# Kernel optimization log

Hardware: AMD Instinct MI355X
Metric: run time of the kernel (lower is better)

## Reference

```python
import jax, jax.numpy as jnp
import numpy as np

B, S, Nv, D, DF, H = 8, 1024, 768, 512, 2048, 8
DH = D // H
EPS = 1e-5


def _layernorm(x, g, b):
    mu = jnp.mean(x, axis=-1, keepdims=True)
    var = jnp.mean((x - mu) ** 2, axis=-1, keepdims=True)
    return (x - mu) * jax.lax.rsqrt(var + EPS) * g + b


def _mha(x, Wq, Wk, Wv, Wo):
    b, s, d = x.shape
    q = (x @ Wq).reshape(b, s, H, DH)
    k = (x @ Wk).reshape(b, s, H, DH)
    v = (x @ Wv).reshape(b, s, H, DH)
    scores = jnp.einsum('bqhd,bkhd->bhqk', q, k) / np.sqrt(DH).astype(np.float32)
    a = jax.nn.softmax(scores, axis=-1)
    o = jnp.einsum('bhqk,bkhd->bqhd', a, v).reshape(b, s, d)
    return o @ Wo


def setup_inputs() -> dict:
    key = jax.random.key(0)
    ks = jax.random.split(key, 20)
    sc = 1.0 / np.sqrt(D)
    scf = 1.0 / np.sqrt(DF)
    n = lambda k, shp, s: (jax.random.normal(k, shp, jnp.float32) * s)
    return {
        'x': n(ks[0], (B, S, D), 1.0),
        'idx_emb_1': jax.random.randint(ks[1], (B, Nv), 0, Nv, dtype=jnp.int64) if jax.config.jax_enable_x64 else jax.random.randint(ks[1], (B, Nv), 0, Nv).astype(jnp.int32),
        'idx_pro_1': jax.random.randint(ks[2], (B, Nv), 0, Nv).astype(jnp.int32),
        'N': Nv,
        'Wq1': n(ks[3], (D, D), sc), 'Wk1': n(ks[4], (D, D), sc),
        'Wv1': n(ks[5], (D, D), sc), 'Wo1': n(ks[6], (D, D), sc),
        'Wq2': n(ks[7], (D, D), sc), 'Wk2': n(ks[8], (D, D), sc),
        'Wv2': n(ks[9], (D, D), sc), 'Wo2': n(ks[10], (D, D), sc),
        'w_conv1': n(ks[11], (D, DF), sc), 'b_conv1': jnp.zeros((DF,), jnp.float32),
        'w_conv2': n(ks[12], (DF, D), scf), 'b_conv2': jnp.zeros((D,), jnp.float32),
        'g1': jnp.ones((D,), jnp.float32), 'beta1': jnp.zeros((D,), jnp.float32),
        'g2': jnp.ones((D,), jnp.float32), 'beta2': jnp.zeros((D,), jnp.float32),
    }


def reference(x, idx_emb_1, idx_pro_1, N,
              Wq1, Wk1, Wv1, Wo1, Wq2, Wk2, Wv2, Wo2,
              w_conv1, b_conv1, w_conv2, b_conv2, g1, beta1, g2, beta2):
    # batched gather-reorder of first N tokens; rest pass through
    x_l1 = x.at[:, :N].set(jnp.take_along_axis(x[:, :N], idx_emb_1[:, :, None].astype(jnp.int32), axis=1))
    attn1 = _mha(x_l1, Wq1, Wk1, Wv1, Wo1)
    attn2 = jnp.flip(_mha(jnp.flip(x_l1, axis=1), Wq2, Wk2, Wv2, Wo2), axis=1)
    new_x1 = attn1 + attn2
    x_l2 = new_x1.at[:, :N].set(jnp.take_along_axis(new_x1[:, :N], idx_pro_1[:, :, None].astype(jnp.int32), axis=1))
    x = _layernorm(x + x_l2, g1, beta1)
    # kernel-size-1 Conv1d FFN == pointwise linear (dropout=0, eval mode)
    y = jnp.maximum(x @ w_conv1 + b_conv1, 0.0)
    y = y @ w_conv2 + b_conv2
    out = _layernorm(x + y, g2, beta2)
    return (out, attn1, attn2)
```

## Files before the change

### kernel.cpp

```cpp
#include <hip/hip_runtime.h>
#include <hip/hip_bf16.h>
#include <stdint.h>

#define B_ 8
#define S_ 1024
#define NV_ 768
#define D_ 512
#define DF_ 2048
#define H_ 8
#define DH_ 64
#define BS_ (B_*S_)
#define BSD_ ((size_t)B_*S_*D_)
#define QKVLD 3072

typedef __bf16 bf16x8 __attribute__((ext_vector_type(8)));
typedef float f32x4 __attribute__((ext_vector_type(4)));
typedef float f32x16 __attribute__((ext_vector_type(16)));
typedef __hip_bfloat16 bf16;

__device__ __forceinline__ void async_copy16(const void* g, void* l) {
  __builtin_amdgcn_global_load_lds((const __attribute__((address_space(1))) void*)g,
                                   (__attribute__((address_space(3))) void*)l, 16, 0, 0);
}

__device__ __forceinline__ void stage_tile(const bf16* __restrict__ g, int gRow0, long ldg,
                                           int gCol0, bf16* lds, int rows, int tid) {
  const int totalBytes = rows << 7;
  for (int off = tid * 16; off < totalBytes; off += 4096) {
    const int r = off >> 7;
    const int c = off & 127;
    const int srcByte = c ^ ((r & 7) << 4);
    const bf16* gp = g + (long)(gRow0 + r) * ldg + gCol0 + (srcByte >> 1);
    async_copy16(gp, (char*)lds + off);
  }
}
__device__ __forceinline__ bf16x8 lds_frag(const bf16* base, int row, int kElem) {
  const int byte = (row << 7) + ((kElem << 1) ^ ((row & 7) << 4));
  return *(const bf16x8*)((const char*)base + byte);
}

__device__ __forceinline__ int fswz(int row) {
  return ((((row >> 3) & 3) << 1) | (row & 1)) << 4;
}

#define SCH_BIAS 1064872540.f
template<int BASE>
__device__ __forceinline__ bf16x8 pexp_frag(const f32x16& s) {
  union { unsigned u[4]; bf16x8 b; } r;
#pragma unroll
  for (int e = 0; e < 4; e++) {
    const int i0 = (int)fmaf(s[BASE + 2 * e], 8388608.f, SCH_BIAS);
    const int i1 = (int)fmaf(s[BASE + 2 * e + 1], 8388608.f, SCH_BIAS);
    r.u[e] = __builtin_amdgcn_perm((unsigned)i1, (unsigned)i0, 0x07060302u);
  }
  return r.b;
}

__device__ __forceinline__ bf16x8 ones_frag() {
  union { ushort u[8]; bf16x8 b; } r;
#pragma unroll
  for (int e = 0; e < 8; e++) r.u[e] = 0x3F80;
  return r.b;
}

__device__ __forceinline__ f32x16 zero16() {
  f32x16 z;
#pragma unroll
  for (int i = 0; i < 16; i++) z[i] = 0.f;
  return z;
}

struct WPanel { const float* src; bf16* dst; int srcLd, dstLd; float scale; };
struct WP16 { WPanel p[16]; };
__global__ __launch_bounds__(256) void wtrans16_kernel(WP16 ws) {
  __shared__ float tile[32][33];
  const WPanel pa = ws.p[blockIdx.z];
  const int tx = threadIdx.x, ty = threadIdx.y;
  const int n0 = blockIdx.x * 32, k0 = blockIdx.y * 32;
#pragma unroll
  for (int i = 0; i < 4; i++)
    tile[ty + i * 8][tx] = pa.src[(long)(k0 + ty + i * 8) * pa.srcLd + n0 + tx];
  __syncthreads();
#pragma unroll
  for (int i = 0; i < 4; i++)
    pa.dst[(long)(n0 + ty + i * 8) * pa.dstLd + k0 + tx] =
        __float2bfloat16(tile[tx][ty + i * 8] * pa.scale);
}

__global__ __launch_bounds__(256) void vtrans_kernel(const bf16* __restrict__ qkv,
                                                     bf16* __restrict__ vtb) {
  __shared__ bf16 tile[32][33];
  const int tx = threadIdx.x, ty = threadIdx.y;
  const int s0 = blockIdx.x * 32, d0 = blockIdx.y * 32;
  const int z = blockIdx.z;
  const int set = z >> 6, bh = z & 63;
  const bf16* sp = qkv + (long)(bh >> 3) * S_ * QKVLD + set * 1536 + 1024 + (bh & 7) * 64;
  bf16* dp = vtb + (long)z * DH_ * S_;
#pragma unroll
  for (int i = 0; i < 4; i++) tile[ty + i * 8][tx] = sp[(long)(s0 + ty + i * 8) * QKVLD + d0 + tx];
  __syncthreads();
  const int c = s0 + tx;
  const int cp = (c & ~12) | ((c & 4) << 1) | ((c & 8) >> 1);
#pragma unroll
  for (int i = 0; i < 4; i++) dp[(long)(d0 + ty + i * 8) * S_ + cp] = tile[tx][ty + i * 8];
}

__global__ __launch_bounds__(256) void gather_cvt_kernel(const float* __restrict__ x,
                                                         const int* __restrict__ idx,
                                                         const int* __restrict__ Np,
                                                         bf16* __restrict__ out) {
  const int N = *Np;
  const int row = blockIdx.x * 2 + (threadIdx.x >> 7);
  const int t = threadIdx.x & 127;
  const int b = row >> 10, s = row & 1023;
  const int src = (s < N) ? idx[b * NV_ + s] : s;
  const float4 v = *(const float4*)(x + ((long)b * S_ + src) * D_ + t * 4);
  ushort4 u;
  u.x = (ushort)__bfloat16_as_ushort(__float2bfloat16(v.x));
  u.y = (ushort)__bfloat16_as_ushort(__float2bfloat16(v.y));
  u.z = (ushort)__bfloat16_as_ushort(__float2bfloat16(v.z));
  u.w = (ushort)__bfloat16_as_ushort(__float2bfloat16(v.w));
  *(ushort4*)(out + (long)row * D_ + t * 4) = u;
}

template<int BM, int BN, int MR, int NR, int OUTF, int BIAS, int RELU>
__global__ __launch_bounds__(256) void gemm_bt(const bf16* __restrict__ A, long lda, long sAz,
                                               const bf16* __restrict__ Bt, long sBz,
                                               const float* __restrict__ bias,
                                               void* __restrict__ C, long ldc, long sCz,
                                               int K) {
  constexpr int WC = BN / (NR * 16);
  constexpr int WR = BM / (MR * 16);
  static_assert(WR * WC == 4, "4 waves");
  __shared__ bf16 As[BM * 64];
  __shared__ bf16 Bs[BN * 64];
  const int tid = threadIdx.x;
  const int lane = tid & 63, wave = tid >> 6;
  const int wr = wave / WC, wc = wave % WC;
  const int g = lane >> 4, lr = lane & 15;
  const int m0 = blockIdx.x * BM, n0 = blockIdx.y * BN;
  const int z = blockIdx.z;
  A += (long)z * sAz;
  Bt += (long)z * sBz;

  f32x4 acc[MR][NR];
#pragma unroll
  for (int m = 0; m < MR; m++)
#pragma unroll
    for (int n = 0; n < NR; n++) acc[m][n] = (f32x4){0.f, 0.f, 0.f, 0.f};

  for (int kt = 0; kt < K; kt += 64) {
    stage_tile(A, m0, lda, kt, As, BM, tid);
    stage_tile(Bt, n0, K, kt, Bs, BN, tid);
    __syncthreads();
#pragma unroll
    for (int ks = 0; ks < 64; ks += 32) {
      const int kk = ks + g * 8;
      bf16x8 aF[MR], bF[NR];
#pragma unroll
      for (int m = 0; m < MR; m++) aF[m] = lds_frag(As, wr * (MR * 16) + m * 16 + lr, kk);
#pragma unroll
      for (int n = 0; n < NR; n++) bF[n] = lds_frag(Bs, wc * (NR * 16) + n * 16 + lr, kk);
#pragma unroll
      for (int m = 0; m < MR; m++)
#pragma unroll
        for (int n = 0; n < NR; n++)
          acc[m][n] = __builtin_amdgcn_mfma_f32_16x16x32_bf16(aF[m], bF[n], acc[m][n], 0, 0, 0);
    }
    __syncthreads();
  }

#pragma unroll
  for (int m = 0; m < MR; m++) {
#pragma unroll
    for (int n = 0; n < NR; n++) {
      const int row = m0 + wr * (MR * 16) + m * 16 + g * 4;
      const int col = n0 + wc * (NR * 16) + n * 16 + lr;
      const float bv = BIAS ? bias[col] : 0.f;
#pragma unroll
      for (int r = 0; r < 4; r++) {
        float v = acc[m][n][r] + bv;
        if (RELU) v = fmaxf(v, 0.f);
        if (OUTF) ((float*)C)[(long)z * sCz + (long)(row + r) * ldc + col] = v;
        else ((bf16*)C)[(long)z * sCz + (long)(row + r) * ldc + col] = __float2bfloat16(v);
      }
    }
  }
}

__global__ __launch_bounds__(256, 4) void flash_kernel(bf16* __restrict__ qkv,
                                                       const bf16* __restrict__ vtb) {
  __shared__ char lds[32768];
  const int tid = threadIdx.x;
  const int lane = tid & 63, warp = tid >> 6;
  const int qlo = lane & 31, hi = lane >> 5;

  const int bid = (int)blockIdx.x;
  const int swz = (bid & 7) * 128 + (bid >> 3);
  const int qt = swz & 7;
  const int sbh = swz >> 3;
  const int set = sbh >> 6;
  const int b = (sbh >> 3) & 7, h = sbh & 7;

  bf16* Qp = qkv + (long)b * S_ * QKVLD + set * 1536 + h * DH_;
  const bf16* Kp = Qp + 512;
  const bf16* Vp = vtb + (long)sbh * DH_ * S_;

  const int r0 = tid >> 3;
  const int cb = (tid & 7) << 4;
  const int sb = cb ^ fswz(r0);
  char* const ld0 = lds + tid * 16;

  {
    const bf16* qS = Qp + (long)(qt * 128 + r0) * QKVLD + (sb >> 1);
    async_copy16(qS, ld0);
    async_copy16(qS + 32 * QKVLD, ld0 + 4096);
    async_copy16(qS + 64 * QKVLD, ld0 + 8192);
    async_copy16(qS + 96 * QKVLD, ld0 + 12288);
  }
  const bf16* kS = Kp + (long)r0 * QKVLD + (sb >> 1);
  const bf16* vS = Vp + (long)r0 * S_ + (sb >> 1);
  async_copy16(kS, ld0 + 16384);
  async_copy16(kS + 32 * QKVLD, ld0 + 16384 + 4096);
  async_copy16(vS, ld0 + 16384 + 8192);
  async_copy16(vS + 32 * S_, ld0 + 16384 + 12288);
  __syncthreads();

  const int qrow = warp * 32 + qlo;
  const int qrb = (qrow << 7) | fswz(qrow);
  bf16x8 qFh[4];
#pragma unroll
  for (int d4 = 0; d4 < 4; d4++)
    qFh[d4] = *(const bf16x8*)(lds + (qrb ^ (d4 * 32 + hi * 16)));
  __syncthreads();

  kS += 64 * QKVLD; vS += 64;
  async_copy16(kS, ld0);
  async_copy16(kS + 32 * QKVLD, ld0 + 4096);
  async_copy16(vS, ld0 + 8192);
  async_copy16(vS + 32 * S_, ld0 + 12288);

  f32x16 oAcc0 = zero16(), oAcc1 = zero16(), sAcc = zero16();
  const bf16x8 onesF = ones_frag();
  const int rb = (qlo << 7) | fswz(qlo);

  for (int t = 0; t < 16; t++) {
    const int bb = ((t & 1) ^ 1) << 14;
    const int kbase = bb + rb;
    const int vbase = bb + 8192 + rb;

    f32x16 s0 = zero16(), s1 = zero16();
    __builtin_amdgcn_s_setprio(1);
#pragma unroll
    for (int d4 = 0; d4 < 4; d4++) {
      const int kc2 = d4 * 32 + hi * 16;
      const bf16x8 kf0 = *(const bf16x8*)(lds + (kbase ^ kc2));
      const bf16x8 kf1 = *(const bf16x8*)(lds + ((kbase + 4096) ^ kc2));
      s0 = __builtin_amdgcn_mfma_f32_32x32x16_bf16(kf0, qFh[d4], s0, 0, 0, 0);
      s1 = __builtin_amdgcn_mfma_f32_32x32x16_bf16(kf1, qFh[d4], s1, 0, 0, 0);
    }
    __builtin_amdgcn_s_setprio(0);

    __builtin_amdgcn_s_setprio(1);
    {
      const bf16x8 pa0 = pexp_frag<0>(s0);
      oAcc0 = __builtin_amdgcn_mfma_f32_32x32x16_bf16(pa0, *(const bf16x8*)(lds + ((vbase) ^ (hi * 16))), oAcc0, 0, 0, 0);
      oAcc1 = __builtin_amdgcn_mfma_f32_32x32x16_bf16(pa0, *(const bf16x8*)(lds + ((vbase + 4096) ^ (hi * 16))), oAcc1, 0, 0, 0);
      sAcc = __builtin_amdgcn_mfma_f32_32x32x16_bf16(pa0, onesF, sAcc, 0, 0, 0);
      const bf16x8 pa1 = pexp_frag<8>(s0);
      oAcc0 = __builtin_amdgcn_mfma_f32_32x32x16_bf16(pa1, *(const bf16x8*)(lds + ((vbase) ^ (32 + hi * 16))), oAcc0, 0, 0, 0);
      oAcc1 = __builtin_amdgcn_mfma_f32_32x32x16_bf16(pa1, *(const bf16x8*)(lds + ((vbase + 4096) ^ (32 + hi * 16))), oAcc1, 0, 0, 0);
      sAcc = __builtin_amdgcn_mfma_f32_32x32x16_bf16(pa1, onesF, sAcc, 0, 0, 0);
      const bf16x8 pa2 = pexp_frag<0>(s1);
      oAcc0 = __builtin_amdgcn_mfma_f32_32x32x16_bf16(pa2, *(const bf16x8*)(lds + ((vbase) ^ (64 + hi * 16))), oAcc0, 0, 0, 0);
      oAcc1 = __builtin_amdgcn_mfma_f32_32x32x16_bf16(pa2, *(const bf16x8*)(lds + ((vbase + 4096) ^ (64 + hi * 16))), oAcc1, 0, 0, 0);
      sAcc = __builtin_amdgcn_mfma_f32_32x32x16_bf16(pa2, onesF, sAcc, 0, 0, 0);
      const bf16x8 pa3 = pexp_frag<8>(s1);
      oAcc0 = __builtin_amdgcn_mfma_f32_32x32x16_bf16(pa3, *(const bf16x8*)(lds + ((vbase) ^ (96 + hi * 16))), oAcc0, 0, 0, 0);
      oAcc1 = __builtin_amdgcn_mfma_f32_32x32x16_bf16(pa3, *(const bf16x8*)(lds + ((vbase + 4096) ^ (96 + hi * 16))), oAcc1, 0, 0, 0);
      sAcc = __builtin_amdgcn_mfma_f32_32x32x16_bf16(pa3, onesF, sAcc, 0, 0, 0);
    }
    __builtin_amdgcn_s_setprio(0);

    __syncthreads();
    if (t + 2 < 16) {
      kS += 64 * QKVLD; vS += 64;
      char* dst = ld0 + bb;
      async_copy16(kS, dst);
      async_copy16(kS + 32 * QKVLD, dst + 4096);
      async_copy16(vS, dst + 8192);
      async_copy16(vS + 32 * S_, dst + 12288);
    }
  }

#pragma unroll
  for (int r = 0; r < 16; r++) {
    const int q = (r & 3) + 8 * (r >> 2) + 4 * hi;
    const float linv = 1.f / sAcc[r];
    bf16* op = Qp + (long)(qt * 128 + warp * 32 + q) * QKVLD;
    op[qlo] = __float2bfloat16(oAcc0[r] * linv);
    op[32 + qlo] = __float2bfloat16(oAcc1[r] * linv);
  }
}

__global__ __launch_bounds__(256) void fuse1_kernel(const float* __restrict__ x,
                                                    const float* __restrict__ a1,
                                                    const float* __restrict__ a2,
                                                    const int* __restrict__ idx,
                                                    const int* __restrict__ Np,
                                                    const float* __restrict__ gw,
                                                    const float* __restrict__ bw,
                                                    bf16* __restrict__ xlnB) {
  const int N = *Np;
  const int row = blockIdx.x * 4 + (threadIdx.x >> 6);
  const int lane = threadIdx.x & 63;
  const int b = row >> 10, s = row & 1023;
  const int j = (s < N) ? idx[b * NV_ + s] : s;
  const float* xp = x + (long)row * D_ + lane * 8;
  const float* p1 = a1 + ((long)b * S_ + j) * D_ + lane * 8;
  const float* p2 = a2 + ((long)b * S_ + j) * D_ + lane * 8;
  float v[8];
  float sum = 0.f;
#pragma unroll
  for (int q = 0; q < 2; q++) {
    const float4 t = ((const float4*)xp)[q];
    const float4 u = ((const float4*)p1)[q];
    const float4 w = ((const float4*)p2)[q];
    v[q * 4 + 0] = t.x + u.x + w.x; v[q * 4 + 1] = t.y + u.y + w.y;
    v[q * 4 + 2] = t.z + u.z + w.z; v[q * 4 + 3] = t.w + u.w + w.w;
  }
#pragma unroll
  for (int i = 0; i < 8; i++) sum += v[i];
#pragma unroll
  for (int o = 1; o < 64; o <<= 1) sum += __shfl_xor(sum, o, 64);
  const float mu = sum * (1.f / D_);
  float var = 0.f;
#pragma unroll
  for (int i = 0; i < 8; i++) { const float t = v[i] - mu; var += t * t; }
#pragma unroll
  for (int o = 1; o < 64; o <<= 1) var += __shfl_xor(var, o, 64);
  const float rs = rsqrtf(var * (1.f / D_) + 1e-5f);
#pragma unroll
  for (int i = 0; i < 8; i++) {
    const int d = lane * 8 + i;
    xlnB[(long)row * D_ + d] = __float2bfloat16((v[i] - mu) * rs * gw[d] + bw[d]);
  }
}

__global__ __launch_bounds__(256) void fuse2_kernel(const bf16* __restrict__ xlnB,
                                                    const bf16* __restrict__ ybf,
                                                    const float* __restrict__ gw,
                                                    const float* __restrict__ bw,
                                                    float* __restrict__ out) {
  const int row = blockIdx.x * 4 + (threadIdx.x >> 6);
  const int lane = threadIdx.x & 63;
  const bf16* xp = xlnB + (long)row * D_ + lane * 8;
  const bf16* yp = ybf + (long)row * D_ + lane * 8;
  float v[8];
  float sum = 0.f;
#pragma unroll
  for (int i = 0; i < 8; i++) {
    v[i] = __bfloat162float(xp[i]) + __bfloat162float(yp[i]);
    sum += v[i];
  }
#pragma unroll
  for (int o = 1; o < 64; o <<= 1) sum += __shfl_xor(sum, o, 64);
  const float mu = sum * (1.f / D_);
  float var = 0.f;
#pragma unroll
  for (int i = 0; i < 8; i++) { const float t = v[i] - mu; var += t * t; }
#pragma unroll
  for (int o = 1; o < 64; o <<= 1) var += __shfl_xor(var, o, 64);
  const float rs = rsqrtf(var * (1.f / D_) + 1e-5f);
#pragma unroll
  for (int i = 0; i < 8; i++) {
    const int d = lane * 8 + i;
    out[(long)row * D_ + d] = (v[i] - mu) * rs * gw[d] + bw[d];
  }
}

extern "C" void kernel_launch(void* const* d_in, const int* in_sizes, int n_in,
                              void* d_out, int out_size, void* d_ws, size_t ws_size,
                              hipStream_t stream) {
  const float* x   = (const float*)d_in[0];
  const int* idx1  = (const int*)d_in[1];
  const int* idx2  = (const int*)d_in[2];
  const int* Np    = (const int*)d_in[3];
  const float* b_conv1 = (const float*)d_in[13];
  const float* b_conv2 = (const float*)d_in[15];
  const float* g1    = (const float*)d_in[16];
  const float* beta1 = (const float*)d_in[17];
  const float* g2    = (const float*)d_in[18];
  const float* beta2 = (const float*)d_in[19];

  float* outp  = (float*)d_out;
  float* attn1 = outp + BSD_;

  const size_t DD = (size_t)D_ * D_;
  char* w = (char*)d_ws;
  bf16* wT  = (bf16*)w;
  bf16* w1T = wT + 8 * DD;
  bf16* w2T = w1T + (size_t)DF_ * D_;
  bf16* qkv = (bf16*)(w + (8ll << 20));
  bf16* xl1 = (bf16*)(w + (56ll << 20));
  bf16* vtb = (bf16*)(w + (56ll << 20));
  bf16* xlnB = (bf16*)(w + (56ll << 20));
  bf16* ffn = (bf16*)(w + (8ll << 20));
  bf16* ybf = (bf16*)(w + (40ll << 20));

  WP16 wp;
  const float* attnW[8] = {(const float*)d_in[4], (const float*)d_in[5], (const float*)d_in[6],
                           (const float*)d_in[8], (const float*)d_in[9], (const float*)d_in[10],
                           (const float*)d_in[7], (const float*)d_in[11]};
  for (int z = 0; z < 8; z++) {
    wp.p[z].src = attnW[z];
    wp.p[z].dst = wT + (size_t)z * DD;
    wp.p[z].srcLd = D_; wp.p[z].dstLd = D_;
    wp.p[z].scale = (z == 0 || z == 3) ? 0.1803368801f : 1.f;
  }
  for (int j = 0; j < 4; j++) {
    wp.p[8 + j].src = (const float*)d_in[12] + 512 * j;
    wp.p[8 + j].dst = w1T + (size_t)(512 * j) * D_;
    wp.p[8 + j].srcLd = DF_; wp.p[8 + j].dstLd = D_;
    wp.p[8 + j].scale = 1.f;
  }
  for (int j = 0; j < 4; j++) {
    wp.p[12 + j].src = (const float*)d_in[14] + (size_t)(512 * j) * D_;
    wp.p[12 + j].dst = w2T + 512 * j;
    wp.p[12 + j].srcLd = D_; wp.p[12 + j].dstLd = DF_;
    wp.p[12 + j].scale = 1.f;
  }

  const dim3 tb(32, 8);
  wtrans16_kernel<<<dim3(16, 16, 16), tb, 0, stream>>>(wp);

  gather_cvt_kernel<<<BS_ / 2, 256, 0, stream>>>(x, idx1, Np, xl1);

  gemm_bt<128, 128, 4, 4, 0, 0, 0><<<dim3(BS_ / 128, QKVLD / 128, 1), 256, 0, stream>>>(
      xl1, D_, 0, wT, 0, nullptr, qkv, QKVLD, 0, D_);

  vtrans_kernel<<<dim3(S_ / 32, DH_ / 32, 128), tb, 0, stream>>>(qkv, vtb);

  flash_kernel<<<1024, 256, 0, stream>>>(qkv, vtb);

  gemm_bt<128, 128, 4, 4, 1, 0, 0><<<dim3(BS_ / 128, D_ / 128, 2), 256, 0, stream>>>(
      qkv, QKVLD, 1536, wT + 6 * DD, (long)DD, nullptr, attn1, D_, (long)BSD_, D_);

  fuse1_kernel<<<BS_ / 4, 256, 0, stream>>>(x, attn1, attn1 + BSD_, idx2, Np, g1, beta1, xlnB);

  gemm_bt<128, 128, 4, 4, 0, 1, 1><<<dim3(BS_ / 128, DF_ / 128, 1), 256, 0, stream>>>(
      xlnB, D_, 0, w1T, 0, b_conv1, ffn, DF_, 0, D_);
  gemm_bt<128, 64, 4, 2, 0, 1, 0><<<dim3(BS_ / 128, D_ / 64, 1), 256, 0, stream>>>(
      ffn, DF_, 0, w2T, 0, b_conv2, ybf, D_, 0, DF_);

  fuse2_kernel<<<BS_ / 4, 256, 0, stream>>>(xlnB, ybf, g2, beta2, outp);
}
```

Baseline: 196.5 us.

## Triple-buffer K/V tiles in flash attention with explicit vmcnt waits

The flash attention kernel moves from double to triple buffering of K/V tiles. Q gets its own LDS region, and the loop waits on vmcnt counters plus a raw s_barrier instead of __syncthreads, so the load for tile t+2 is issued before computing tile t. This is meant to hide global-to-LDS latency and drop one barrier per iteration. In exchange LDS grows to 48KB and occupancy drops from 4 to 3 blocks per CU.

```diff
diff --git a/kernel.cpp b/kernel.cpp
--- a/kernel.cpp
+++ b/kernel.cpp
@@ -17,6 +17,8 @@
 typedef float f32x4 __attribute__((ext_vector_type(4)));
 typedef float f32x16 __attribute__((ext_vector_type(16)));
 typedef __hip_bfloat16 bf16;
+
+#define VMCNT(n) asm volatile("s_waitcnt vmcnt(" #n ")" ::: "memory")
 
 __device__ __forceinline__ void async_copy16(const void* g, void* l) {
   __builtin_amdgcn_global_load_lds((const __attribute__((address_space(1))) void*)g,
@@ -188,9 +190,9 @@
   }
 }
 
-__global__ __launch_bounds__(256, 4) void flash_kernel(bf16* __restrict__ qkv,
+__global__ __launch_bounds__(256, 3) void flash_kernel(bf16* __restrict__ qkv,
                                                        const bf16* __restrict__ vtb) {
-  __shared__ char lds[32768];
+  __shared__ char lds[49152];
   const int tid = threadIdx.x;
   const int lane = tid & 63, warp = tid >> 6;
   const int qlo = lane & 31, hi = lane >> 5;
@@ -207,47 +209,62 @@
   const bf16* Vp = vtb + (long)sbh * DH_ * S_;
 
   const int r0 = tid >> 3;
-  const int cb = (tid & 7) << 4;
-  const int sb = cb ^ fswz(r0);
+  const int cbyt = (tid & 7) << 4;
+  const int sb = cbyt ^ fswz(r0);
   char* const ld0 = lds + tid * 16;
 
   {
     const bf16* qS = Qp + (long)(qt * 128 + r0) * QKVLD + (sb >> 1);
-    async_copy16(qS, ld0);
-    async_copy16(qS + 32 * QKVLD, ld0 + 4096);
-    async_copy16(qS + 64 * QKVLD, ld0 + 8192);
-    async_copy16(qS + 96 * QKVLD, ld0 + 12288);
+    async_copy16(qS, ld0 + 32768);
+    async_copy16(qS + 32 * QKVLD, ld0 + 32768 + 4096);
+    async_copy16(qS + 64 * QKVLD, ld0 + 32768 + 8192);
+    async_copy16(qS + 96 * QKVLD, ld0 + 32768 + 12288);
   }
   const bf16* kS = Kp + (long)r0 * QKVLD + (sb >> 1);
   const bf16* vS = Vp + (long)r0 * S_ + (sb >> 1);
+  async_copy16(kS, ld0);
+  async_copy16(kS + 32 * QKVLD, ld0 + 4096);
+  async_copy16(vS, ld0 + 8192);
+  async_copy16(vS + 32 * S_, ld0 + 12288);
+  kS += 64 * QKVLD; vS += 64;
   async_copy16(kS, ld0 + 16384);
   async_copy16(kS + 32 * QKVLD, ld0 + 16384 + 4096);
   async_copy16(vS, ld0 + 16384 + 8192);
   async_copy16(vS + 32 * S_, ld0 + 16384 + 12288);
-  __syncthreads();
+  kS += 64 * QKVLD; vS += 64;
+
+  VMCNT(8);
+  __builtin_amdgcn_s_barrier();
 
   const int qrow = warp * 32 + qlo;
-  const int qrb = (qrow << 7) | fswz(qrow);
+  const int qrb = 32768 + ((qrow << 7) | fswz(qrow));
   bf16x8 qFh[4];
 #pragma unroll
   for (int d4 = 0; d4 < 4; d4++)
     qFh[d4] = *(const bf16x8*)(lds + (qrb ^ (d4 * 32 + hi * 16)));
-  __syncthreads();
-
-  kS += 64 * QKVLD; vS += 64;
-  async_copy16(kS, ld0);
-  async_copy16(kS + 32 * QKVLD, ld0 + 4096);
-  async_copy16(vS, ld0 + 8192);
-  async_copy16(vS + 32 * S_, ld0 + 12288);
+  asm volatile("s_waitcnt lgkmcnt(0)" ::: "memory");
+  __builtin_amdgcn_sched_barrier(0);
 
   f32x16 oAcc0 = zero16(), oAcc1 = zero16(), sAcc = zero16();
   const bf16x8 onesF = ones_frag();
   const int rb = (qlo << 7) | fswz(qlo);
 
+  int cb = 0;
+#pragma unroll 1
   for (int t = 0; t < 16; t++) {
-    const int bb = ((t & 1) ^ 1) << 14;
-    const int kbase = bb + rb;
-    const int vbase = bb + 8192 + rb;
+    if (t == 15) { VMCNT(0); } else { VMCNT(4); }
+    __builtin_amdgcn_s_barrier();
+    __builtin_amdgcn_sched_barrier(0);
+    if (t + 2 < 16) {
+      char* dst = ld0 + (cb == 0 ? 32768 : cb - 16384);
+      async_copy16(kS, dst);
+      async_copy16(kS + 32 * QKVLD, dst + 4096);
+      async_copy16(vS, dst + 8192);
+      async_copy16(vS + 32 * S_, dst + 12288);
+      kS += 64 * QKVLD; vS += 64;
+    }
+    const int kbase = cb + rb;
+    const int vbase = cb + 8192 + rb;
 
     f32x16 s0 = zero16(), s1 = zero16();
     __builtin_amdgcn_s_setprio(1);
@@ -282,15 +299,7 @@
     }
     __builtin_amdgcn_s_setprio(0);
 
-    __syncthreads();
-    if (t + 2 < 16) {
-      kS += 64 * QKVLD; vS += 64;
-      char* dst = ld0 + bb;
-      async_copy16(kS, dst);
-      async_copy16(kS + 32 * QKVLD, dst + 4096);
-      async_copy16(vS, dst + 8192);
-      async_copy16(vS + 32 * S_, dst + 12288);
-    }
+    cb = (cb == 32768) ? 0 : cb + 16384;
   }
 
 #pragma unroll
```

New measurement: 196.8 us. No clear change (+0.2%).
